# Optimization experiments

Measured on AMD Instinct MI355X. Metric: run time of the kernel, lower is better.

Reference implementation:

```python
import jax, jax.numpy as jnp
import numpy as np

B, T, I = 64, 512, 128
H, R, DA, C = 256, 20, 50, 10

def setup_inputs() -> dict:
    key = jax.random.key(0)
    ks = jax.random.split(key, 8)
    s = 0.05
    return {
        "x": jax.random.normal(ks[0], (B, T, I), dtype=jnp.float32),
        "W_ih": jax.random.normal(ks[1], (I, 4 * H), dtype=jnp.float32) * s,
        "W_hh": jax.random.normal(ks[2], (H, 4 * H), dtype=jnp.float32) * s,
        "b": jnp.zeros((4 * H,), dtype=jnp.float32),
        "W1": jax.random.normal(ks[3], (DA, I), dtype=jnp.float32) * s,
        "b1": jnp.zeros((DA,), dtype=jnp.float32),
        "W2": jax.random.normal(ks[4], (R, DA), dtype=jnp.float32) * s,
        "b2": jnp.zeros((R,), dtype=jnp.float32),
        "Wfc": jax.random.normal(ks[5], (C, H), dtype=jnp.float32) * s,
        "bfc": jnp.zeros((C,), dtype=jnp.float32),
    }

def reference(x, W_ih, W_hh, b, W1, b1, W2, b2, Wfc, bfc):
    # Dropout is identity (eval mode). Attention scores for all timesteps at once.
    bsz, seq, inp = x.shape
    hid = W_hh.shape[0]
    r = W2.shape[0]
    # scores: [B, T, r]
    S = jnp.tanh(jnp.einsum('bti,di->btd', x, W1) + b1)
    S = jnp.einsum('btd,rd->btr', S, W2) + b2
    # Prefix softmax over time via cumulative sums (softmax shift-invariant,
    # use global max over time per (b, r) for stability).
    E = jnp.exp(S - jnp.max(S, axis=1, keepdims=True))          # [B, T, r]
    denom = jnp.cumsum(E, axis=1)                               # [B, T, r]
    numer = jnp.cumsum(E[:, :, :, None] * x[:, :, None, :], axis=1)  # [B, T, r, I]
    M = jnp.mean(numer / denom[:, :, :, None], axis=2)          # [B, T, I]
    # Precompute input contribution to gates for all steps.
    gx = jnp.einsum('bti,ig->btg', M, W_ih) + b                 # [B, T, 4H]
    h0 = jnp.ones((bsz, hid), dtype=x.dtype)
    c0 = jnp.ones((bsz, hid), dtype=x.dtype)

    def step(carry, g_x):
        h, c = carry
        g = g_x + h @ W_hh
        i_t = jax.nn.sigmoid(g[:, :hid])
        f_t = jax.nn.sigmoid(g[:, hid:2 * hid])
        g_t = jnp.tanh(g[:, 2 * hid:3 * hid])
        o_t = jax.nn.sigmoid(g[:, 3 * hid:])
        c = f_t * c + i_t * g_t
        h = o_t * jnp.tanh(c)
        return (h, c), None

    (h_T, _), _ = jax.lax.scan(step, (h0, c0), jnp.swapaxes(gx, 0, 1))
    logits = h_T @ Wfc.T + bfc                                  # [B, C]
    return jax.nn.softmax(logits, axis=1)
```

## Files before the change

### kernel.cpp

```cpp
#include <hip/hip_runtime.h>
#include <hip/hip_fp16.h>

#define B_   64
#define T_   512
#define I_   128
#define H_   256
#define G4_  1024
#define R_   20
#define DA_  50
#define C_   10

typedef _Float16 half2_t __attribute__((ext_vector_type(2)));
typedef _Float16 half8_t __attribute__((ext_vector_type(8)));

__device__ __forceinline__ float fsigmoid(float x) {
  return __fdividef(1.0f, 1.0f + __expf(-x));
}
__device__ __forceinline__ float ftanh(float x) {
  return 1.0f - __fdividef(2.0f, __expf(2.0f * x) + 1.0f);
}

__global__ __launch_bounds__(256) void k0_pack(const float* __restrict__ Whh,
                                               half2_t* __restrict__ Wq) {
  int idx = blockIdx.x * 256 + threadIdx.x;
  int g = idx & 1023, k2 = idx >> 10;
  half2_t h;
  h.x = (_Float16)Whh[(2 * k2) * G4_ + g];
  h.y = (_Float16)Whh[(2 * k2 + 1) * G4_ + g];
  Wq[g * 128 + k2] = h;
}

__global__ __launch_bounds__(256) void k_init(unsigned long long* __restrict__ Hx) {
  int i = blockIdx.x * 256 + threadIdx.x;
  Hx[i] = 0ull;
}

__global__ __launch_bounds__(256) void k1_scores(const float* __restrict__ x,
                                                 const float* __restrict__ W1,
                                                 const float* __restrict__ b1,
                                                 const float* __restrict__ W2,
                                                 const float* __restrict__ b2,
                                                 float* __restrict__ S) {
  __shared__ float xs[64][129];
  __shared__ float w1s[128][64];
  __shared__ float a1s[64][53];
  int blk = blockIdx.x;
  int tid = threadIdx.x;
  int row0 = blk * 64;
  const float4* xv = (const float4*)(x + (size_t)row0 * I_);
#pragma unroll
  for (int ch = 0; ch < 8; ch++) {
    int fidx = ch * 256 + tid;
    int r = fidx >> 5, k4 = (fidx & 31) << 2;
    float4 f = xv[fidx];
    xs[r][k4] = f.x; xs[r][k4 + 1] = f.y; xs[r][k4 + 2] = f.z; xs[r][k4 + 3] = f.w;
  }
  const float4* w1v = (const float4*)W1;
#pragma unroll
  for (int ch = 0; ch < 7; ch++) {
    int fidx = ch * 256 + tid;
    if (fidx < 1600) {
      int d = fidx >> 5, k4 = (fidx & 31) << 2;
      float4 f = w1v[fidx];
      w1s[k4][d] = f.x; w1s[k4 + 1][d] = f.y; w1s[k4 + 2][d] = f.z; w1s[k4 + 3][d] = f.w;
    }
  }
  __syncthreads();
  int ty = tid >> 4, tx = tid & 15;
  float acc[4][4] = {};
#pragma unroll 4
  for (int k = 0; k < I_; k++) {
    float a0 = xs[4 * ty][k], a1 = xs[4 * ty + 1][k];
    float a2 = xs[4 * ty + 2][k], a3 = xs[4 * ty + 3][k];
    float4 bq = *(const float4*)&w1s[k][tx << 2];
    acc[0][0] += a0 * bq.x; acc[0][1] += a0 * bq.y; acc[0][2] += a0 * bq.z; acc[0][3] += a0 * bq.w;
    acc[1][0] += a1 * bq.x; acc[1][1] += a1 * bq.y; acc[1][2] += a1 * bq.z; acc[1][3] += a1 * bq.w;
    acc[2][0] += a2 * bq.x; acc[2][1] += a2 * bq.y; acc[2][2] += a2 * bq.z; acc[2][3] += a2 * bq.w;
    acc[3][0] += a3 * bq.x; acc[3][1] += a3 * bq.y; acc[3][2] += a3 * bq.z; acc[3][3] += a3 * bq.w;
  }
#pragma unroll
  for (int i = 0; i < 4; i++) {
#pragma unroll
    for (int j = 0; j < 4; j++) {
      int col = (tx << 2) + j;
      if (col < DA_) a1s[4 * ty + i][col] = tanhf(acc[i][j] + b1[col]);
    }
  }
  __syncthreads();
  int row = tid & 63, rq = tid >> 6;
  int bt = row0 + row;
  int b = bt >> 9, t = bt & 511;
#pragma unroll
  for (int m = 0; m < 5; m++) {
    int r = rq + (m << 2);
    float acc2 = b2[r];
#pragma unroll 10
    for (int d = 0; d < DA_; d++) acc2 += a1s[row][d] * W2[r * DA_ + d];
    S[((size_t)(b * R_ + r)) * T_ + t] = acc2;
  }
}

__global__ __launch_bounds__(64) void k2_prefix(const float* __restrict__ S,
                                                float* __restrict__ E,
                                                float* __restrict__ invd) {
  int br = blockIdx.x;
  int l = threadIdx.x;
  const float* Sr = S + (size_t)br * T_;
  float v[8];
  float m = -1e30f;
#pragma unroll
  for (int c = 0; c < 8; c++) {
    v[c] = Sr[c * 64 + l];
    m = fmaxf(m, v[c]);
  }
#pragma unroll
  for (int off = 32; off; off >>= 1) m = fmaxf(m, __shfl_xor(m, off));
  float carry = 0.f;
  for (int c = 0; c < 8; c++) {
    float e = expf(v[c] - m);
    float s = e;
#pragma unroll
    for (int off = 1; off < 64; off <<= 1) {
      float u = __shfl_up(s, off);
      if (l >= off) s += u;
    }
    E[(size_t)br * T_ + c * 64 + l] = e;
    invd[(size_t)br * T_ + c * 64 + l] = 1.f / (carry + s);
    carry += __shfl(s, 63);
  }
}

__global__ __launch_bounds__(128) void k3a(const float* __restrict__ x,
                                           const float* __restrict__ E,
                                           float* __restrict__ P) {
  int b = blockIdx.x >> 3, c = blockIdx.x & 7;
  int i = threadIdx.x;
  int t0 = c * 64;
  __shared__ float es[2][R_];
  float acc[R_];
#pragma unroll
  for (int r = 0; r < R_; r++) acc[r] = 0.f;
  float rE = 0.f;
  if (i < R_) rE = E[((size_t)(b * R_ + i)) * T_ + t0];
  const float* xb = x + (size_t)b * T_ * I_;
  float xv = xb[(size_t)t0 * I_ + i];
  int buf = 0;
  for (int tt = 0; tt < 64; tt++) {
    if (i < R_) es[buf][i] = rE;
    __syncthreads();
    if (tt + 1 < 64) {
      if (i < R_) rE = E[((size_t)(b * R_ + i)) * T_ + t0 + tt + 1];
    }
    float xcur = xv;
    if (tt + 1 < 64) xv = xb[(size_t)(t0 + tt + 1) * I_ + i];
#pragma unroll
    for (int r = 0; r < R_; r++) acc[r] += es[buf][r] * xcur;
    buf ^= 1;
  }
#pragma unroll
  for (int r = 0; r < R_; r++)
    P[(size_t)((b * 8 + c) * R_ + r) * I_ + i] = acc[r];
}

__global__ __launch_bounds__(256) void k3b(float* __restrict__ P) {
  int gid = blockIdx.x * 256 + threadIdx.x;
  int i = gid & 127;
  int r = (gid >> 7) % R_;
  int b = gid / (R_ * I_);
  float s = 0.f;
#pragma unroll
  for (int c = 0; c < 8; c++) {
    size_t idx = (size_t)((b * 8 + c) * R_ + r) * I_ + i;
    float v = P[idx];
    P[idx] = s;
    s += v;
  }
}

__global__ __launch_bounds__(128) void k3c(const float* __restrict__ x,
                                           const float* __restrict__ E,
                                           const float* __restrict__ invd,
                                           const float* __restrict__ P,
                                           float* __restrict__ M) {
  int b = blockIdx.x >> 3, c = blockIdx.x & 7;
  int i = threadIdx.x;
  int t0 = c * 64;
  __shared__ float es[2][R_], ds[2][R_];
  float acc[R_];
#pragma unroll
  for (int r = 0; r < R_; r++)
    acc[r] = P[(size_t)((b * 8 + c) * R_ + r) * I_ + i];
  float rE = 0.f, rD = 0.f;
  if (i < R_)
    rE = E[((size_t)(b * R_ + i)) * T_ + t0];
  else if (i < 2 * R_)
    rD = invd[((size_t)(b * R_ + (i - R_))) * T_ + t0];
  const float* xb = x + (size_t)b * T_ * I_;
  float xv = xb[(size_t)t0 * I_ + i];
  int buf = 0;
  for (int tt = 0; tt < 64; tt++) {
    if (i < R_) es[buf][i] = rE;
    else if (i < 2 * R_) ds[buf][i - R_] = rD;
    __syncthreads();
    if (tt + 1 < 64) {
      if (i < R_)
        rE = E[((size_t)(b * R_ + i)) * T_ + t0 + tt + 1];
      else if (i < 2 * R_)
        rD = invd[((size_t)(b * R_ + (i - R_))) * T_ + t0 + tt + 1];
    }
    float xcur = xv;
    if (tt + 1 < 64) xv = xb[(size_t)(t0 + tt + 1) * I_ + i];
    float s = 0.f;
#pragma unroll
    for (int r = 0; r < R_; r++) {
      acc[r] += es[buf][r] * xcur;
      s += acc[r] * ds[buf][r];
    }
    M[(size_t)b * T_ * I_ + (size_t)(t0 + tt) * I_ + i] = s * (1.0f / R_);
    buf ^= 1;
  }
}

__global__ __launch_bounds__(256) void k4_gemm(const float* __restrict__ Mm,
                                               const float* __restrict__ Wih,
                                               const float* __restrict__ bg,
                                               __half* __restrict__ gx) {
  __shared__ float As[I_][64];
  __shared__ float Bs[I_][64];
  int row0 = blockIdx.x * 64, col0 = blockIdx.y * 64;
  int tid = threadIdx.x;
#pragma unroll
  for (int ch = 0; ch < 8; ch++) {
    int fidx = ch * 256 + tid;
    int r = fidx >> 5;
    int kk = (fidx & 31) << 2;
    float4 f = ((const float4*)(Mm + (size_t)(row0 + r) * I_))[fidx & 31];
    As[kk + 0][r] = f.x;
    As[kk + 1][r] = f.y;
    As[kk + 2][r] = f.z;
    As[kk + 3][r] = f.w;
  }
#pragma unroll
  for (int ch = 0; ch < 8; ch++) {
    int fidx = ch * 256 + tid;
    int k = fidx >> 4;
    int c4 = (fidx & 15) << 2;
    float4 f = *((const float4*)(Wih + (size_t)k * G4_ + col0 + c4));
    *((float4*)&Bs[k][c4]) = f;
  }
  __syncthreads();
  int ty = tid >> 4, tx = tid & 15;
  float acc[4][4] = {};
#pragma unroll 4
  for (int k = 0; k < I_; k++) {
    float4 a = *((float4*)&As[k][ty << 2]);
    float4 bq = *((float4*)&Bs[k][tx << 2]);
    acc[0][0] += a.x * bq.x; acc[0][1] += a.x * bq.y; acc[0][2] += a.x * bq.z; acc[0][3] += a.x * bq.w;
    acc[1][0] += a.y * bq.x; acc[1][1] += a.y * bq.y; acc[1][2] += a.y * bq.z; acc[1][3] += a.y * bq.w;
    acc[2][0] += a.z * bq.x; acc[2][1] += a.z * bq.y; acc[2][2] += a.z * bq.z; acc[2][3] += a.z * bq.w;
    acc[3][0] += a.w * bq.x; acc[3][1] += a.w * bq.y; acc[3][2] += a.w * bq.z; acc[3][3] += a.w * bq.w;
  }
#pragma unroll
  for (int ii = 0; ii < 4; ii++) {
#pragma unroll
    for (int jj = 0; jj < 4; jj++) {
      int row = row0 + (ty << 2) + ii;
      int col = col0 + (tx << 2) + jj;
      gx[(size_t)row * G4_ + col] = __float2half(acc[ii][jj] + bg[col]);
    }
  }
}

union WREG {
  unsigned u[64];
  half2_t h[64];
  uint4 q[16];
};

__global__ __launch_bounds__(512, 2) void k5_lstm(
    const __half* __restrict__ gx, const half2_t* __restrict__ Wq,
    unsigned long long* __restrict__ Hx, float* __restrict__ hT) {
  int b = blockIdx.x & 63;
  int p = blockIdx.x >> 6;
  int tid = threadIdx.x;
  int wave = tid >> 6;
  int lane = tid & 63;
  int kh = lane & 1;
  int gate = (lane >> 1) & 3;
  int uw = lane >> 3;
  int u = wave * 8 + uw;
  int gcol = gate * H_ + p * 64 + u;

  __shared__ __align__(16) unsigned hsU[2][128];

  int qi = tid >> 5;
  int q_ = qi + (qi >= p ? 1 : 0);
  int d_ = tid & 31;

  WREG w;
  {
    const uint4* wp = (const uint4*)(Wq + (size_t)gcol * 128 + kh * 64);
#pragma unroll
    for (int i = 0; i < 16; i++) w.q[i] = wp[i];
  }
#pragma unroll
  for (int j = 0; j < 64; j++) asm volatile("" : "+v"(w.u[j]));

  float cstate = 1.0f;
  const __half* gxb = gx + (size_t)b * T_ * G4_;

  for (int t = 0; t < T_; t++) {
    float gxv = 0.f;
    if (!kh) gxv = (float)gxb[(size_t)t * G4_ + gcol];

    if (t == 0) {
      if (tid < 128) hsU[0][tid] = 0x3C003C00u;
    } else if (tid < 96) {
      const unsigned long long* src =
          Hx + ((size_t)(t & 1) * 64 + b) * 128 + q_ * 32 + d_;
      unsigned long long v;
      do {
        v = __hip_atomic_load(src, __ATOMIC_RELAXED, __HIP_MEMORY_SCOPE_AGENT);
      } while ((unsigned)(v >> 32) != (unsigned)t);
      hsU[t & 1][q_ * 32 + d_] = (unsigned)v;
    }
    __syncthreads();

    const half2_t* hb = (const half2_t*)hsU[t & 1] + kh * 64;
    float a0 = 0.f, a1 = 0.f, a2 = 0.f, a3 = 0.f;
#pragma unroll
    for (int i = 0; i < 16; i++) {
      half8_t hv = *(const half8_t*)(hb + i * 4);
      half2_t h0 = ((half2_t*)&hv)[0], h1 = ((half2_t*)&hv)[1];
      half2_t h2 = ((half2_t*)&hv)[2], h3 = ((half2_t*)&hv)[3];
      a0 = __builtin_amdgcn_fdot2(w.h[4 * i + 0], h0, a0, false);
      a1 = __builtin_amdgcn_fdot2(w.h[4 * i + 1], h1, a1, false);
      a2 = __builtin_amdgcn_fdot2(w.h[4 * i + 2], h2, a2, false);
      a3 = __builtin_amdgcn_fdot2(w.h[4 * i + 3], h3, a3, false);
    }
    float s = (a0 + a1) + (a2 + a3);
    s += __shfl_xor(s, 1);
    s += gxv;

    float f1 = __shfl_down(s, 2);
    float f2 = __shfl_down(s, 4);
    float f3 = __shfl_down(s, 6);
    unsigned hu = 0;
    if ((lane & 7) == 0) {
      float vi = fsigmoid(s);
      float vf = fsigmoid(f1);
      float vg = ftanh(f2);
      float vo = fsigmoid(f3);
      cstate = vf * cstate + vi * vg;
      float h = vo * ftanh(cstate);
      hu = (unsigned)__half_as_ushort(__float2half(h));
      if (t == T_ - 1) hT[b * H_ + p * 64 + u] = h;
    }
    unsigned hup = (unsigned)__shfl_down((int)hu, 8);
    if ((lane & 15) == 0 && (t + 1) < T_) {
      unsigned h2pack = hu | (hup << 16);
      int slot = p * 32 + wave * 4 + (lane >> 4);
      unsigned long long pkt =
          (unsigned long long)h2pack |
          ((unsigned long long)(unsigned)(t + 1) << 32);
      unsigned long long* dst =
          Hx + ((size_t)((t + 1) & 1) * 64 + b) * 128 + slot;
      __hip_atomic_store(dst, pkt, __ATOMIC_RELAXED, __HIP_MEMORY_SCOPE_AGENT);
      hsU[(t + 1) & 1][slot] = h2pack;
    }
  }
}

__global__ __launch_bounds__(64) void k6_head(const float* __restrict__ hT,
                                              const float* __restrict__ Wfc,
                                              const float* __restrict__ bfc,
                                              float* __restrict__ out) {
  int b = blockIdx.x, l = threadIdx.x;
  const float* h = hT + b * H_;
  float p[C_];
#pragma unroll
  for (int c = 0; c < C_; c++) p[c] = 0.f;
#pragma unroll
  for (int q = 0; q < 4; q++) {
    float hv = h[q * 64 + l];
#pragma unroll
    for (int c = 0; c < C_; c++) p[c] += hv * Wfc[c * H_ + q * 64 + l];
  }
#pragma unroll
  for (int c = 0; c < C_; c++)
    for (int off = 32; off; off >>= 1) p[c] += __shfl_xor(p[c], off);
  if (l == 0) {
    float m = -1e30f, e[C_], sum = 0.f;
    for (int c = 0; c < C_; c++) { p[c] += bfc[c]; m = fmaxf(m, p[c]); }
    for (int c = 0; c < C_; c++) { e[c] = expf(p[c] - m); sum += e[c]; }
    for (int c = 0; c < C_; c++) out[b * C_ + c] = e[c] / sum;
  }
}

extern "C" void kernel_launch(void* const* d_in, const int* in_sizes, int n_in,
                              void* d_out, int out_size, void* d_ws, size_t ws_size,
                              hipStream_t stream) {
  const float* x   = (const float*)d_in[0];
  const float* Wih = (const float*)d_in[1];
  const float* Whh = (const float*)d_in[2];
  const float* bg  = (const float*)d_in[3];
  const float* W1  = (const float*)d_in[4];
  const float* b1  = (const float*)d_in[5];
  const float* W2  = (const float*)d_in[6];
  const float* b2  = (const float*)d_in[7];
  const float* Wfc = (const float*)d_in[8];
  const float* bfc = (const float*)d_in[9];
  float* out = (float*)d_out;

  float* wsf = (float*)d_ws;
  unsigned long long* Hx = (unsigned long long*)wsf;
  float* S    = wsf;
  float* E    = wsf + 655360;
  float* INVD = wsf + 1310720;
  float* Mm   = wsf + 1966080;
  float* hT   = wsf + 6160384;
  half2_t* Wq = (half2_t*)(wsf + 6176768);
  __half* gx  = (__half*)(wsf + 6307840);
  float* P    = wsf + 6307840;

  hipLaunchKernelGGL(k0_pack,   dim3(512),     dim3(256), 0, stream, Whh, Wq);
  hipLaunchKernelGGL(k1_scores, dim3(512),     dim3(256), 0, stream, x, W1, b1, W2, b2, S);
  hipLaunchKernelGGL(k2_prefix, dim3(B_ * R_), dim3(64),  0, stream, S, E, INVD);
  hipLaunchKernelGGL(k3a,       dim3(512),     dim3(128), 0, stream, x, E, P);
  hipLaunchKernelGGL(k3b,       dim3(640),     dim3(256), 0, stream, P);
  hipLaunchKernelGGL(k3c,       dim3(512),     dim3(128), 0, stream, x, E, INVD, P, Mm);
  hipLaunchKernelGGL(k4_gemm,   dim3(512, 16), dim3(256), 0, stream, Mm, Wih, bg, gx);
  hipLaunchKernelGGL(k_init,    dim3(64),      dim3(256), 0, stream, Hx);
  hipLaunchKernelGGL(k5_lstm,   dim3(256),     dim3(512), 0, stream, gx, Wq, Hx, hT);
  hipLaunchKernelGGL(k6_head,   dim3(B_),      dim3(64),  0, stream, hT, Wfc, bfc, out);
}
```

Baseline: 1.141 ms.

## Run each batch's LSTM recurrence in one 1024-thread block without cross-block flags

```diff
diff --git a/kernel.cpp b/kernel.cpp
--- a/kernel.cpp
+++ b/kernel.cpp
@@ -28,11 +28,6 @@
   h.x = (_Float16)Whh[(2 * k2) * G4_ + g];
   h.y = (_Float16)Whh[(2 * k2 + 1) * G4_ + g];
   Wq[g * 128 + k2] = h;
-}
-
-__global__ __launch_bounds__(256) void k_init(unsigned long long* __restrict__ Hx) {
-  int i = blockIdx.x * 256 + threadIdx.x;
-  Hx[i] = 0ull;
 }
 
 __global__ __launch_bounds__(256) void k1_scores(const float* __restrict__ x,
@@ -271,66 +266,48 @@
   }
 }
 
-union WREG {
-  unsigned u[64];
-  half2_t h[64];
-  uint4 q[16];
-};
-
-__global__ __launch_bounds__(512, 2) void k5_lstm(
+__global__ __launch_bounds__(1024) void k5_lstm(
     const __half* __restrict__ gx, const half2_t* __restrict__ Wq,
-    unsigned long long* __restrict__ Hx, float* __restrict__ hT) {
-  int b = blockIdx.x & 63;
-  int p = blockIdx.x >> 6;
+    float* __restrict__ hT) {
+  int b = blockIdx.x;
   int tid = threadIdx.x;
+  int lane = tid & 63;
   int wave = tid >> 6;
-  int lane = tid & 63;
-  int kh = lane & 1;
-  int gate = (lane >> 1) & 3;
-  int uw = lane >> 3;
-  int u = wave * 8 + uw;
-  int gcol = gate * H_ + p * 64 + u;
-
-  __shared__ __align__(16) unsigned hsU[2][128];
-
-  int qi = tid >> 5;
-  int q_ = qi + (qi >= p ? 1 : 0);
-  int d_ = tid & 31;
-
-  WREG w;
+  int gate = lane & 3;
+  int u = wave * 16 + (lane >> 2);
+  int gcol = gate * H_ + u;
+
+  __shared__ __align__(16) __half hs[2][H_];
+
+  union WREG {
+    unsigned u32[128];
+    half2_t h[128];
+    uint4 q[32];
+  } w;
   {
-    const uint4* wp = (const uint4*)(Wq + (size_t)gcol * 128 + kh * 64);
-#pragma unroll
-    for (int i = 0; i < 16; i++) w.q[i] = wp[i];
-  }
-#pragma unroll
-  for (int j = 0; j < 64; j++) asm volatile("" : "+v"(w.u[j]));
+    const uint4* wp = (const uint4*)(Wq + (size_t)gcol * 128);
+#pragma unroll
+    for (int i = 0; i < 32; i++) w.q[i] = wp[i];
+  }
+#pragma unroll
+  for (int j = 0; j < 128; j++) asm volatile("" : "+v"(w.u32[j]));
+
+  if (tid < H_) hs[0][tid] = __float2half(1.0f);
+  __syncthreads();
 
   float cstate = 1.0f;
-  const __half* gxb = gx + (size_t)b * T_ * G4_;
+  const __half* gxb = gx + (size_t)b * T_ * G4_ + gcol;
+  float gxv = (float)gxb[0];
 
   for (int t = 0; t < T_; t++) {
-    float gxv = 0.f;
-    if (!kh) gxv = (float)gxb[(size_t)t * G4_ + gcol];
-
-    if (t == 0) {
-      if (tid < 128) hsU[0][tid] = 0x3C003C00u;
-    } else if (tid < 96) {
-      const unsigned long long* src =
-          Hx + ((size_t)(t & 1) * 64 + b) * 128 + q_ * 32 + d_;
-      unsigned long long v;
-      do {
-        v = __hip_atomic_load(src, __ATOMIC_RELAXED, __HIP_MEMORY_SCOPE_AGENT);
-      } while ((unsigned)(v >> 32) != (unsigned)t);
-      hsU[t & 1][q_ * 32 + d_] = (unsigned)v;
-    }
-    __syncthreads();
-
-    const half2_t* hb = (const half2_t*)hsU[t & 1] + kh * 64;
+    float nextgx = 0.f;
+    if (t + 1 < T_) nextgx = (float)gxb[(size_t)(t + 1) * G4_];
+
+    const half8_t* hb = (const half8_t*)hs[t & 1];
     float a0 = 0.f, a1 = 0.f, a2 = 0.f, a3 = 0.f;
 #pragma unroll
-    for (int i = 0; i < 16; i++) {
-      half8_t hv = *(const half8_t*)(hb + i * 4);
+    for (int i = 0; i < 32; i++) {
+      half8_t hv = hb[i];
       half2_t h0 = ((half2_t*)&hv)[0], h1 = ((half2_t*)&hv)[1];
       half2_t h2 = ((half2_t*)&hv)[2], h3 = ((half2_t*)&hv)[3];
       a0 = __builtin_amdgcn_fdot2(w.h[4 * i + 0], h0, a0, false);
@@ -338,36 +315,23 @@
       a2 = __builtin_amdgcn_fdot2(w.h[4 * i + 2], h2, a2, false);
       a3 = __builtin_amdgcn_fdot2(w.h[4 * i + 3], h3, a3, false);
     }
-    float s = (a0 + a1) + (a2 + a3);
-    s += __shfl_xor(s, 1);
-    s += gxv;
-
-    float f1 = __shfl_down(s, 2);
-    float f2 = __shfl_down(s, 4);
-    float f3 = __shfl_down(s, 6);
-    unsigned hu = 0;
-    if ((lane & 7) == 0) {
+    float s = (a0 + a1) + (a2 + a3) + gxv;
+
+    float f1 = __shfl_down(s, 1);
+    float f2 = __shfl_down(s, 2);
+    float f3 = __shfl_down(s, 3);
+    if (gate == 0) {
       float vi = fsigmoid(s);
       float vf = fsigmoid(f1);
       float vg = ftanh(f2);
       float vo = fsigmoid(f3);
       cstate = vf * cstate + vi * vg;
       float h = vo * ftanh(cstate);
-      hu = (unsigned)__half_as_ushort(__float2half(h));
-      if (t == T_ - 1) hT[b * H_ + p * 64 + u] = h;
-    }
-    unsigned hup = (unsigned)__shfl_down((int)hu, 8);
-    if ((lane & 15) == 0 && (t + 1) < T_) {
-      unsigned h2pack = hu | (hup << 16);
-      int slot = p * 32 + wave * 4 + (lane >> 4);
-      unsigned long long pkt =
-          (unsigned long long)h2pack |
-          ((unsigned long long)(unsigned)(t + 1) << 32);
-      unsigned long long* dst =
-          Hx + ((size_t)((t + 1) & 1) * 64 + b) * 128 + slot;
-      __hip_atomic_store(dst, pkt, __ATOMIC_RELAXED, __HIP_MEMORY_SCOPE_AGENT);
-      hsU[(t + 1) & 1][slot] = h2pack;
-    }
+      hs[(t + 1) & 1][u] = __float2half(h);
+      if (t == T_ - 1) hT[b * H_ + u] = h;
+    }
+    __syncthreads();
+    gxv = nextgx;
   }
 }
 
@@ -413,7 +377,6 @@
   float* out = (float*)d_out;
 
   float* wsf = (float*)d_ws;
-  unsigned long long* Hx = (unsigned long long*)wsf;
   float* S    = wsf;
   float* E    = wsf + 655360;
   float* INVD = wsf + 1310720;
@@ -423,14 +386,13 @@
   __half* gx  = (__half*)(wsf + 6307840);
   float* P    = wsf + 6307840;
 
-  hipLaunchKernelGGL(k0_pack,   dim3(512),     dim3(256), 0, stream, Whh, Wq);
-  hipLaunchKernelGGL(k1_scores, dim3(512),     dim3(256), 0, stream, x, W1, b1, W2, b2, S);
-  hipLaunchKernelGGL(k2_prefix, dim3(B_ * R_), dim3(64),  0, stream, S, E, INVD);
-  hipLaunchKernelGGL(k3a,       dim3(512),     dim3(128), 0, stream, x, E, P);
-  hipLaunchKernelGGL(k3b,       dim3(640),     dim3(256), 0, stream, P);
-  hipLaunchKernelGGL(k3c,       dim3(512),     dim3(128), 0, stream, x, E, INVD, P, Mm);
-  hipLaunchKernelGGL(k4_gemm,   dim3(512, 16), dim3(256), 0, stream, Mm, Wih, bg, gx);
-  hipLaunchKernelGGL(k_init,    dim3(64),      dim3(256), 0, stream, Hx);
-  hipLaunchKernelGGL(k5_lstm,   dim3(256),     dim3(512), 0, stream, gx, Wq, Hx, hT);
-  hipLaunchKernelGGL(k6_head,   dim3(B_),      dim3(64),  0, stream, hT, Wfc, bfc, out);
-}
+  hipLaunchKernelGGL(k0_pack,   dim3(512),     dim3(256),  0, stream, Whh, Wq);
+  hipLaunchKernelGGL(k1_scores, dim3(512),     dim3(256),  0, stream, x, W1, b1, W2, b2, S);
+  hipLaunchKernelGGL(k2_prefix, dim3(B_ * R_), dim3(64),   0, stream, S, E, INVD);
+  hipLaunchKernelGGL(k3a,       dim3(512),     dim3(128),  0, stream, x, E, P);
+  hipLaunchKernelGGL(k3b,       dim3(640),     dim3(256),  0, stream, P);
+  hipLaunchKernelGGL(k3c,       dim3(512),     dim3(128),  0, stream, x, E, INVD, P, Mm);
+  hipLaunchKernelGGL(k4_gemm,   dim3(512, 16), dim3(256),  0, stream, Mm, Wih, bg, gx);
+  hipLaunchKernelGGL(k5_lstm,   dim3(B_),      dim3(1024), 0, stream, gx, Wq, hT);
+  hipLaunchKernelGGL(k6_head,   dim3(B_),      dim3(64),   0, stream, hT, Wfc, bfc, out);
+}
```

After: 2.236 ms. +96.0%, slower.

## Move LSTM recurrent weights from registers to LDS and prefetch next gate input

Applied to the files above, without the earlier changes.

```diff
diff --git a/kernel.cpp b/kernel.cpp
--- a/kernel.cpp
+++ b/kernel.cpp
@@ -11,7 +11,6 @@
 #define C_   10
 
 typedef _Float16 half2_t __attribute__((ext_vector_type(2)));
-typedef _Float16 half8_t __attribute__((ext_vector_type(8)));
 
 __device__ __forceinline__ float fsigmoid(float x) {
   return __fdividef(1.0f, 1.0f + __expf(-x));
@@ -271,13 +270,10 @@
   }
 }
 
-union WREG {
-  unsigned u[64];
-  half2_t h[64];
-  uint4 q[16];
-};
-
-__global__ __launch_bounds__(512, 2) void k5_lstm(
+#define BCH2(u) __builtin_bit_cast(half2_t, (u))
+#define FDOT(w, h, a) __builtin_amdgcn_fdot2(BCH2(w), BCH2(h), (a), false)
+
+__global__ __launch_bounds__(512, 1) void k5_lstm(
     const __half* __restrict__ gx, const half2_t* __restrict__ Wq,
     unsigned long long* __restrict__ Hx, float* __restrict__ hT) {
   int b = blockIdx.x & 63;
@@ -291,52 +287,59 @@
   int u = wave * 8 + uw;
   int gcol = gate * H_ + p * 64 + u;
 
-  __shared__ __align__(16) unsigned hsU[2][128];
+  __shared__ uint4 Wl[16 * 512];
+  __shared__ __align__(16) unsigned hs32[2][128];
+
+  const uint4* wq4 = (const uint4*)Wq;
+#pragma unroll
+  for (int it = 0; it < 16; it++) {
+    int lin = it * 512 + tid;
+    int j = lin & 15;
+    int skh = (lin >> 4) & 1;
+    int suw = (lin >> 5) & 7;
+    int swv = (lin >> 8) & 7;
+    int sgate = lin >> 11;
+    int sgcol = sgate * H_ + p * 64 + swv * 8 + suw;
+    int dst = swv * 64 + suw * 8 + sgate * 2 + skh;
+    Wl[j * 512 + dst] = wq4[sgcol * 32 + skh * 16 + j];
+  }
+  if (tid < 128) hs32[0][tid] = 0x3C003C00u;
+  __syncthreads();
 
   int qi = tid >> 5;
   int q_ = qi + (qi >= p ? 1 : 0);
   int d_ = tid & 31;
 
-  WREG w;
-  {
-    const uint4* wp = (const uint4*)(Wq + (size_t)gcol * 128 + kh * 64);
-#pragma unroll
-    for (int i = 0; i < 16; i++) w.q[i] = wp[i];
-  }
-#pragma unroll
-  for (int j = 0; j < 64; j++) asm volatile("" : "+v"(w.u[j]));
-
   float cstate = 1.0f;
-  const __half* gxb = gx + (size_t)b * T_ * G4_;
+  const __half* gxb = gx + (size_t)b * T_ * G4_ + gcol;
+  float gxv = 0.f;
+  if (!kh) gxv = (float)gxb[0];
 
   for (int t = 0; t < T_; t++) {
-    float gxv = 0.f;
-    if (!kh) gxv = (float)gxb[(size_t)t * G4_ + gcol];
-
-    if (t == 0) {
-      if (tid < 128) hsU[0][tid] = 0x3C003C00u;
-    } else if (tid < 96) {
+    float nextgx = 0.f;
+    if (!kh && t + 1 < T_) nextgx = (float)gxb[(size_t)(t + 1) * G4_];
+
+    if (t > 0 && tid < 96) {
       const unsigned long long* src =
           Hx + ((size_t)(t & 1) * 64 + b) * 128 + q_ * 32 + d_;
       unsigned long long v;
       do {
         v = __hip_atomic_load(src, __ATOMIC_RELAXED, __HIP_MEMORY_SCOPE_AGENT);
       } while ((unsigned)(v >> 32) != (unsigned)t);
-      hsU[t & 1][q_ * 32 + d_] = (unsigned)v;
+      hs32[t & 1][q_ * 32 + d_] = (unsigned)v;
     }
     __syncthreads();
 
-    const half2_t* hb = (const half2_t*)hsU[t & 1] + kh * 64;
+    const uint4* hb = (const uint4*)hs32[t & 1] + kh * 16;
     float a0 = 0.f, a1 = 0.f, a2 = 0.f, a3 = 0.f;
 #pragma unroll
-    for (int i = 0; i < 16; i++) {
-      half8_t hv = *(const half8_t*)(hb + i * 4);
-      half2_t h0 = ((half2_t*)&hv)[0], h1 = ((half2_t*)&hv)[1];
-      half2_t h2 = ((half2_t*)&hv)[2], h3 = ((half2_t*)&hv)[3];
-      a0 = __builtin_amdgcn_fdot2(w.h[4 * i + 0], h0, a0, false);
-      a1 = __builtin_amdgcn_fdot2(w.h[4 * i + 1], h1, a1, false);
-      a2 = __builtin_amdgcn_fdot2(w.h[4 * i + 2], h2, a2, false);
-      a3 = __builtin_amdgcn_fdot2(w.h[4 * i + 3], h3, a3, false);
+    for (int j = 0; j < 16; j++) {
+      uint4 wv = Wl[j * 512 + tid];
+      uint4 hq = hb[j];
+      a0 = FDOT(wv.x, hq.x, a0);
+      a1 = FDOT(wv.y, hq.y, a1);
+      a2 = FDOT(wv.z, hq.z, a2);
+      a3 = FDOT(wv.w, hq.w, a3);
     }
     float s = (a0 + a1) + (a2 + a3);
     s += __shfl_xor(s, 1);
@@ -358,16 +361,17 @@
     }
     unsigned hup = (unsigned)__shfl_down((int)hu, 8);
     if ((lane & 15) == 0 && (t + 1) < T_) {
-      unsigned h2pack = hu | (hup << 16);
+      unsigned pk = hu | (hup << 16);
       int slot = p * 32 + wave * 4 + (lane >> 4);
       unsigned long long pkt =
-          (unsigned long long)h2pack |
+          (unsigned long long)pk |
           ((unsigned long long)(unsigned)(t + 1) << 32);
       unsigned long long* dst =
           Hx + ((size_t)((t + 1) & 1) * 64 + b) * 128 + slot;
       __hip_atomic_store(dst, pkt, __ATOMIC_RELAXED, __HIP_MEMORY_SCOPE_AGENT);
-      hsU[(t + 1) & 1][slot] = h2pack;
-    }
+      hs32[(t + 1) & 1][slot] = pk;
+    }
+    gxv = nextgx;
   }
 }
 
```

After: 1.228 ms. 1.08x slower.
